# Optimization experiments

Measured on AMD Instinct MI355X. Metric: run time of the kernel, lower is better.

## Reference

```python
import jax, jax.numpy as jnp
import numpy as np

B, S, D, H = 2, 2048, 1024, 16
DK = D // H


def setup_inputs() -> dict:
    key = jax.random.key(0)
    ks = jax.random.split(key, 12)
    sc = 0.02
    inp = {
        "q": jax.random.normal(ks[0], (B, S, D), jnp.float32),
        "k": jax.random.normal(ks[1], (B, S, D), jnp.float32),
        "v": jax.random.normal(ks[2], (B, S, D), jnp.float32),
        "mask": jnp.ones((B, S, S), jnp.int32),
        "Wq": jax.random.normal(ks[3], (D, D), jnp.float32) * sc,
        "bq": jnp.zeros((D,), jnp.float32),
        "Wk": jax.random.normal(ks[4], (D, D), jnp.float32) * sc,
        "bk": jnp.zeros((D,), jnp.float32),
        "Wv": jax.random.normal(ks[5], (D, D), jnp.float32) * sc,
        "bv": jnp.zeros((D,), jnp.float32),
        "Wo": jax.random.normal(ks[6], (D, D), jnp.float32) * sc,
        "bo": jnp.zeros((D,), jnp.float32),
    }
    return inp


def _split_heads(x):
    # [B,S,D] -> [B,H,S,DK]
    b, s, _ = x.shape
    return x.reshape(b, s, H, DK).transpose(0, 2, 1, 3)


def reference(q, k, v, mask, Wq, bq, Wk, bk, Wv, bv, Wo, bo):
    qh = _split_heads(q @ Wq.T + bq)
    kh = _split_heads(k @ Wk.T + bk)
    vh = _split_heads(v @ Wv.T + bv)
    scale = 1.0 / jnp.sqrt(jnp.float32(DK))
    scores = jnp.einsum("bhqd,bhkd->bhqk", qh, kh) * scale  # [B,H,S,S]
    scores = jnp.where(mask[:, None, :, :] == 0, jnp.float32(-1e9), scores)
    probs = jax.nn.softmax(scores, axis=-1)  # dropout p=0.0 -> identity
    out = jnp.einsum("bhqk,bhkd->bhqd", probs, vh)  # [B,H,S,DK]
    concat = out.transpose(0, 2, 1, 3).reshape(q.shape[0], -1, D)
    return concat @ Wo.T + bo
```

## Files before the change

### kernel.cpp

```cpp
#include <hip/hip_runtime.h>
#include <stdint.h>

#define Bsz 2
#define Ssz 2048
#define Dsz 1024
#define Hsz 16
#define DKsz 64

typedef __attribute__((ext_vector_type(8))) short sh8;
typedef __attribute__((ext_vector_type(4))) float fx4;
typedef __attribute__((ext_vector_type(16))) float fx16;
typedef __attribute__((ext_vector_type(4))) unsigned ux4;

__device__ __forceinline__ unsigned short f2bf(float x) {
  uint32_t u = __builtin_bit_cast(uint32_t, x);
  uint32_t r = (u + 0x7fffu + ((u >> 16) & 1u)) >> 16;
  return (unsigned short)r;
}

__device__ __forceinline__ fx4 mfma16(sh8 a, sh8 b, fx4 c) {
  return __builtin_amdgcn_mfma_f32_16x16x32_bf16(a, b, c, 0, 0, 0);
}

__device__ __forceinline__ fx16 mfma32(sh8 a, sh8 b, fx16 c) {
  return __builtin_amdgcn_mfma_f32_32x32x16_bf16(a, b, c, 0, 0, 0);
}

__device__ __forceinline__ void g2l16(const void* g, void* l) {
  __builtin_amdgcn_global_load_lds((const __attribute__((address_space(1))) void*)g,
                                   (__attribute__((address_space(3))) void*)l, 16, 0, 0);
}

__device__ __forceinline__ float fexp2(float x) {
#if __has_builtin(__builtin_amdgcn_exp2f)
  return __builtin_amdgcn_exp2f(x);
#else
  return exp2f(x);
#endif
}

__device__ __forceinline__ unsigned cvtpk(float lo, float hi) {
  unsigned r;
  asm("v_cvt_pk_bf16_f32 %0, %1, %2" : "=v"(r) : "v"(lo), "v"(hi));
  return r;
}

__device__ __forceinline__ void plswap(unsigned& a, unsigned& b) {
  asm("v_permlane32_swap_b32 %0, %1" : "+v"(a), "+v"(b));
}

__device__ __forceinline__ void build_pa(const fx16& p, sh8& pa0, sh8& pa1) {
  unsigned w0 = cvtpk(p[0], p[1]), w1 = cvtpk(p[2], p[3]);
  unsigned w2 = cvtpk(p[4], p[5]), w3 = cvtpk(p[6], p[7]);
  unsigned w4 = cvtpk(p[8], p[9]), w5 = cvtpk(p[10], p[11]);
  unsigned w6 = cvtpk(p[12], p[13]), w7 = cvtpk(p[14], p[15]);
  plswap(w0, w2);
  plswap(w1, w3);
  ux4 u0 = {w0, w1, w2, w3};
  pa0 = __builtin_bit_cast(sh8, u0);
  plswap(w4, w6);
  plswap(w5, w7);
  ux4 u1 = {w4, w5, w6, w7};
  pa1 = __builtin_bit_cast(sh8, u1);
}

__global__ __launch_bounds__(256) void convert_kernel(
    const float* __restrict__ wq, const float* __restrict__ wk, const float* __restrict__ wv,
    const float* __restrict__ wo, const int* __restrict__ mask,
    unsigned short* __restrict__ wqb, unsigned short* __restrict__ wkb,
    unsigned short* __restrict__ wvb, unsigned short* __restrict__ wob,
    int* __restrict__ flag) {
  const int NW = Dsz * Dsz / 4;
  const int NC = 4 * NW;
  const int NM = Bsz * Ssz * Ssz / 4;
  const int total = NC + NM;
  int bad = 0;
  for (int i = blockIdx.x * blockDim.x + threadIdx.x; i < total; i += gridDim.x * blockDim.x) {
    if (i >= NC) {
      int4 m = ((const int4*)mask)[i - NC];
      if (m.x == 0 || m.y == 0 || m.z == 0 || m.w == 0) bad = 1;
      continue;
    }
    int t = i / NW, off = i - t * NW;
    const float* src = (t == 0) ? wq : ((t == 1) ? wk : ((t == 2) ? wv : wo));
    unsigned short* dst = (t == 0) ? wqb : ((t == 1) ? wkb : ((t == 2) ? wvb : wob));
    float4 x = ((const float4*)src)[off];
    ushort4 o;
    o.x = f2bf(x.x); o.y = f2bf(x.y); o.z = f2bf(x.z); o.w = f2bf(x.w);
    ((ushort4*)dst)[off] = o;
  }
  if (bad) atomicAnd(flag, 0);
}

__global__ __launch_bounds__(256) void proj_qkv_kernel(
    const float* __restrict__ qf, const float* __restrict__ kf, const float* __restrict__ vf,
    const unsigned short* __restrict__ wqb, const unsigned short* __restrict__ wkb,
    const unsigned short* __restrict__ wvb,
    const float* __restrict__ bq, const float* __restrict__ bk, const float* __restrict__ bv,
    unsigned short* __restrict__ qh, unsigned short* __restrict__ kh,
    unsigned short* __restrict__ vt) {
  __shared__ __align__(16) unsigned short SMEM[17408];
  unsigned short* Ts = SMEM;
  const int z = blockIdx.z;
  const float* X = (z == 0) ? qf : ((z == 1) ? kf : vf);
  const unsigned short* W = (z == 0) ? wqb : ((z == 1) ? wkb : wvb);
  const float* bias = (z == 0) ? bq : ((z == 1) ? bk : bv);
  const int m0 = blockIdx.x * 128, n0 = blockIdx.y * 128;
  const int tid = threadIdx.x, lane = tid & 63, wid = tid >> 6;
  const int wm = wid >> 1, wn = wid & 1;
  const int c = lane & 15, g = lane >> 4;
  fx4 acc[4][4] = {};

  auto LOADA = [&](int k0, float4* a) {
#pragma unroll
    for (int i = 0; i < 4; i++) {
      int c4 = i * 256 + tid;
      a[i] = *(const float4*)(X + (size_t)(m0 + (c4 >> 3)) * Dsz + k0 + (c4 & 7) * 4);
    }
  };
  auto WRITEA = [&](const float4* a, unsigned short* As) {
#pragma unroll
    for (int i = 0; i < 4; i++) {
      int c4 = i * 256 + tid;
      uint2 w;
      w.x = cvtpk(a[i].x, a[i].y);
      w.y = cvtpk(a[i].z, a[i].w);
      *(uint2*)&As[(c4 >> 3) * 32 + (c4 & 7) * 4] = w;
    }
  };
  auto G2LB = [&](int k0, unsigned short* Bs) {
#pragma unroll
    for (int i = 0; i < 2; i++) {
      int e = i * 256 + tid;
      g2l16(W + (size_t)(n0 + (e >> 2)) * Dsz + k0 + (e & 3) * 8,
            (char*)Bs + (size_t)(i * 256 + wid * 64) * 16);
    }
  };
  auto COMPUTE = [&](const unsigned short* As, const unsigned short* Bs) {
    sh8 af[4], bfr[4];
#pragma unroll
    for (int m = 0; m < 4; m++)
      af[m] = *(const sh8*)&As[(wm * 64 + m * 16 + c) * 32 + g * 8];
#pragma unroll
    for (int n = 0; n < 4; n++)
      bfr[n] = *(const sh8*)&Bs[(wn * 64 + n * 16 + c) * 32 + g * 8];
#pragma unroll
    for (int m = 0; m < 4; m++)
#pragma unroll
      for (int n = 0; n < 4; n++)
        acc[m][n] = mfma16(af[m], bfr[n], acc[m][n]);
  };

  float4 aA[4], aB[4];
  LOADA(0, aA);
  G2LB(0, SMEM + 8192);
  WRITEA(aA, SMEM);
  __syncthreads();
#pragma unroll 1
  for (int j = 0; j < 16; j++) {
    const int k0 = j * 64;
    if (k0 + 32 < Dsz) { LOADA(k0 + 32, aB); G2LB(k0 + 32, SMEM + 12288); }
    COMPUTE(SMEM, SMEM + 8192);
    if (k0 + 32 < Dsz) WRITEA(aB, SMEM + 4096);
    __syncthreads();
    if (k0 + 64 < Dsz) { LOADA(k0 + 64, aA); G2LB(k0 + 64, SMEM + 8192); }
    if (k0 + 32 < Dsz) COMPUTE(SMEM + 4096, SMEM + 12288);
    if (k0 + 64 < Dsz) WRITEA(aA, SMEM);
    __syncthreads();
  }

  const float CE = 0.18033688011112042f;
  if (z < 2) {
    unsigned short* O = (z == 0) ? qh : kh;
    const float sc = (z == 0) ? CE : 1.0f;
#pragma unroll
    for (int n = 0; n < 4; n++) {
      int j = n0 + wn * 64 + n * 16 + c;
      float bj = bias[j];
      int h = j >> 6, dk = j & 63;
#pragma unroll
      for (int m = 0; m < 4; m++)
#pragma unroll
        for (int r = 0; r < 4; r++) {
          int i = m0 + wm * 64 + m * 16 + g * 4 + r;
          int b = i >> 11, s = i & 2047;
          O[(((size_t)(b * Hsz + h) * Ssz + s) << 6) + dk] = f2bf((acc[m][n][r] + bj) * sc);
        }
    }
  } else {
#pragma unroll
    for (int n = 0; n < 4; n++) {
      int nl = wn * 64 + n * 16 + c;
      float bj = bias[n0 + nl];
#pragma unroll
      for (int m = 0; m < 4; m++)
#pragma unroll
        for (int r = 0; r < 4; r++) {
          int ml = wm * 64 + m * 16 + g * 4 + r;
          Ts[nl * 136 + ml] = f2bf(acc[m][n][r] + bj);
        }
    }
    __syncthreads();
    int b = m0 >> 11, sbase = m0 & 2047;
#pragma unroll
    for (int it = 0; it < 8; it++) {
      int ch = it * 256 + tid;
      int row = ch >> 4, off = ch & 15;
      sh8 dv = *(const sh8*)&Ts[row * 136 + off * 8];
      int j = n0 + row;
      int h = j >> 6, dk = j & 63;
      *(sh8*)&vt[(size_t)((b * Hsz + h) * DKsz + dk) * Ssz + sbase + off * 8] = dv;
    }
  }
}

__global__ __launch_bounds__(512, 4) void attn_kernel(
    const unsigned short* __restrict__ qh, const unsigned short* __restrict__ kh,
    const unsigned short* __restrict__ vt, const int* __restrict__ mask,
    const int* __restrict__ flag, unsigned short* __restrict__ concat) {
  __shared__ __align__(16) unsigned short SM[2][2][2][4096];
  const int tid = threadIdx.x, lane = tid & 63, wid = tid >> 6;
  const int grp = wid >> 2, w4 = wid & 3;
  const int fid = blockIdx.y * gridDim.x + blockIdx.x;
  const int logical = (fid & 7) * 64 + (fid >> 3);
  const int bh = logical >> 4, qblk = logical & 15;
  const int b = bh >> 4, h = bh & 15;
  const int q0 = qblk * 128 + w4 * 32;
  const int c = lane & 31, hi = lane >> 5;
  const int cs = c & 7;
  const int kvbase = grp * (Ssz / 2);
  const unsigned short* Qb = qh + ((size_t)bh * Ssz + q0) * DKsz;
  const unsigned short* Kb = kh + (size_t)bh * Ssz * DKsz;
  const unsigned short* Vb = vt + (size_t)bh * DKsz * Ssz;
  const int ch0 = w4 * 128 + lane;
  const int ch1 = ch0 + 64;
  const int r0 = ch0 >> 3, sl0 = (ch0 & 7) ^ (r0 & 7);
  const int r1 = ch1 >> 3, sl1 = (ch1 & 7) ^ (r1 & 7);
  const int koff0 = r0 * DKsz + sl0 * 8, koff1 = r1 * DKsz + sl1 * 8;
  const size_t voff0 = (size_t)r0 * Ssz + sl0 * 8, voff1 = (size_t)r1 * Ssz + sl1 * 8;

  sh8 qf[4];
#pragma unroll
  for (int ks = 0; ks < 4; ks++)
    qf[ks] = *(const sh8*)&Qb[(size_t)c * DKsz + ks * 16 + hi * 8];
  const bool allones = (flag[0] != 0);
  float lsum = 0.f;
  fx16 o0 = {}, o1 = {};

  auto STAGE = [&](int bufi, int kv0) {
    const unsigned short* ksrc = Kb + (size_t)kv0 * DKsz;
    char* kdst = (char*)&SM[0][grp][bufi][0] + w4 * 2048;
    g2l16(ksrc + koff0, kdst);
    g2l16(ksrc + koff1, kdst + 1024);
    const unsigned short* vsrc = Vb + kv0;
    char* vdst = (char*)&SM[1][grp][bufi][0] + w4 * 2048;
    g2l16(vsrc + voff0, vdst);
    g2l16(vsrc + voff1, vdst + 1024);
  };

  const int NT = (Ssz / 2) / 64;
  STAGE(0, kvbase);
  asm volatile("s_waitcnt vmcnt(0)" ::: "memory");
  __builtin_amdgcn_s_barrier();
  asm volatile("" ::: "memory");

  for (int t = 0; t < NT; ++t) {
    const int cur = t & 1;
    const int kv0 = kvbase + t * 64;
    if (t + 1 < NT) STAGE(cur ^ 1, kv0 + 64);
    const unsigned short* Kt = &SM[0][grp][cur][0];
    const unsigned short* Vt = &SM[1][grp][cur][0];
    fx16 s0 = {}, s1 = {};
    __builtin_amdgcn_s_setprio(1);
#pragma unroll
    for (int ks = 0; ks < 4; ks++) {
      int sl = (2 * ks + hi) ^ cs;
      sh8 ka = *(const sh8*)&Kt[(c * 8 + sl) * 8];
      sh8 kb2 = *(const sh8*)&Kt[((32 + c) * 8 + sl) * 8];
      s0 = mfma32(ka, qf[ks], s0);
      s1 = mfma32(kb2, qf[ks], s1);
    }
    __builtin_amdgcn_s_setprio(0);
    if (!allones) {
      const int* mrow = mask + ((size_t)b * Ssz + (q0 + c)) * Ssz + kv0;
#pragma unroll
      for (int r = 0; r < 16; r++) {
        int kv = (r & 3) + 8 * (r >> 2) + 4 * hi;
        if (mrow[kv] == 0) s0[r] = -1e9f;
        if (mrow[32 + kv] == 0) s1[r] = -1e9f;
      }
    }
    fx16 p0v, p1v;
#pragma unroll
    for (int r = 0; r < 16; r++) {
      p0v[r] = fexp2(s0[r]);
      p1v[r] = fexp2(s1[r]);
    }
    sh8 pa[4];
    build_pa(p0v, pa[0], pa[1]);
    build_pa(p1v, pa[2], pa[3]);
    __builtin_amdgcn_s_setprio(1);
#pragma unroll
    for (int ks = 0; ks < 4; ks++) {
      int sl = (2 * ks + hi) ^ cs;
      sh8 v0f = *(const sh8*)&Vt[(c * 8 + sl) * 8];
      sh8 v1f = *(const sh8*)&Vt[((32 + c) * 8 + sl) * 8];
      o0 = mfma32(v0f, pa[ks], o0);
      o1 = mfma32(v1f, pa[ks], o1);
    }
    __builtin_amdgcn_s_setprio(0);
    float sm[16];
#pragma unroll
    for (int r = 0; r < 16; r++) sm[r] = p0v[r] + p1v[r];
#pragma unroll
    for (int w = 8; w >= 1; w >>= 1)
#pragma unroll
      for (int r = 0; r < w; r++) sm[r] += sm[r + w];
    lsum += sm[0];
    asm volatile("s_waitcnt vmcnt(0)" ::: "memory");
    __builtin_amdgcn_s_barrier();
    asm volatile("" ::: "memory");
  }

  float* CB = (float*)&SM[0][0][0][0];
  float* CBl = CB + 4 * 32 * 68;
  if (grp == 1) {
#pragma unroll
    for (int k4 = 0; k4 < 4; k4++) {
      fx4 a = {o0[4 * k4], o0[4 * k4 + 1], o0[4 * k4 + 2], o0[4 * k4 + 3]};
      *(fx4*)&CB[(w4 * 32 + c) * 68 + 8 * k4 + 4 * hi] = a;
      fx4 bvv = {o1[4 * k4], o1[4 * k4 + 1], o1[4 * k4 + 2], o1[4 * k4 + 3]};
      *(fx4*)&CB[(w4 * 32 + c) * 68 + 32 + 8 * k4 + 4 * hi] = bvv;
    }
    CBl[w4 * 64 + hi * 32 + c] = lsum;
  }
  __syncthreads();
  if (grp == 0) {
#pragma unroll
    for (int k4 = 0; k4 < 4; k4++) {
      fx4 a = *(const fx4*)&CB[(w4 * 32 + c) * 68 + 8 * k4 + 4 * hi];
      o0[4 * k4] += a[0]; o0[4 * k4 + 1] += a[1]; o0[4 * k4 + 2] += a[2]; o0[4 * k4 + 3] += a[3];
      fx4 bvv = *(const fx4*)&CB[(w4 * 32 + c) * 68 + 32 + 8 * k4 + 4 * hi];
      o1[4 * k4] += bvv[0]; o1[4 * k4 + 1] += bvv[1]; o1[4 * k4 + 2] += bvv[2]; o1[4 * k4 + 3] += bvv[3];
    }
    lsum += CBl[w4 * 64 + hi * 32 + c];
    lsum += __shfl_xor(lsum, 32);
    float linv = 1.0f / lsum;
    unsigned short* Ob = concat + ((size_t)b * Ssz + q0 + c) * Dsz + h * DKsz;
#pragma unroll
    for (int rg = 0; rg < 4; rg++) {
      ushort4 w;
      w.x = f2bf(o0[rg * 4 + 0] * linv);
      w.y = f2bf(o0[rg * 4 + 1] * linv);
      w.z = f2bf(o0[rg * 4 + 2] * linv);
      w.w = f2bf(o0[rg * 4 + 3] * linv);
      *(ushort4*)&Ob[8 * rg + 4 * hi] = w;
      ushort4 w2;
      w2.x = f2bf(o1[rg * 4 + 0] * linv);
      w2.y = f2bf(o1[rg * 4 + 1] * linv);
      w2.z = f2bf(o1[rg * 4 + 2] * linv);
      w2.w = f2bf(o1[rg * 4 + 3] * linv);
      *(ushort4*)&Ob[32 + 8 * rg + 4 * hi] = w2;
    }
  }
}

__global__ __launch_bounds__(256) void outproj_kernel(
    const unsigned short* __restrict__ Xc, const unsigned short* __restrict__ wob,
    const float* __restrict__ bo, float* __restrict__ out) {
  __shared__ __align__(16) unsigned short As[128 * 32];
  __shared__ __align__(16) unsigned short Bs[128 * 32];
  const int m0 = blockIdx.x * 128, n0 = blockIdx.y * 128;
  const int tid = threadIdx.x, lane = tid & 63, wid = tid >> 6;
  const int wm = wid >> 1, wn = wid & 1;
  const int c = lane & 15, g = lane >> 4;
  fx4 acc[4][4] = {};
  for (int k0 = 0; k0 < Dsz; k0 += 32) {
#pragma unroll
    for (int i = 0; i < 2; i++) {
      int e = i * 256 + tid;
      g2l16(Xc + (size_t)(m0 + (e >> 2)) * Dsz + k0 + (e & 3) * 8,
            (char*)As + (size_t)(i * 256 + wid * 64) * 16);
      g2l16(wob + (size_t)(n0 + (e >> 2)) * Dsz + k0 + (e & 3) * 8,
            (char*)Bs + (size_t)(i * 256 + wid * 64) * 16);
    }
    __syncthreads();
    sh8 af[4], bfr[4];
#pragma unroll
    for (int m = 0; m < 4; m++)
      af[m] = *(const sh8*)&As[(wm * 64 + m * 16 + c) * 32 + g * 8];
#pragma unroll
    for (int n = 0; n < 4; n++)
      bfr[n] = *(const sh8*)&Bs[(wn * 64 + n * 16 + c) * 32 + g * 8];
#pragma unroll
    for (int m = 0; m < 4; m++)
#pragma unroll
      for (int n = 0; n < 4; n++)
        acc[m][n] = mfma16(af[m], bfr[n], acc[m][n]);
    __syncthreads();
  }
#pragma unroll
  for (int n = 0; n < 4; n++) {
    int j = n0 + wn * 64 + n * 16 + c;
    float bj = bo[j];
#pragma unroll
    for (int m = 0; m < 4; m++)
#pragma unroll
      for (int r = 0; r < 4; r++) {
        int i = m0 + wm * 64 + m * 16 + g * 4 + r;
        out[(size_t)i * Dsz + j] = acc[m][n][r] + bj;
      }
  }
}

extern "C" void kernel_launch(void* const* d_in, const int* in_sizes, int n_in,
                              void* d_out, int out_size, void* d_ws, size_t ws_size,
                              hipStream_t stream) {
  const float* q = (const float*)d_in[0];
  const float* k = (const float*)d_in[1];
  const float* v = (const float*)d_in[2];
  const int* mask = (const int*)d_in[3];
  const float* Wq = (const float*)d_in[4];
  const float* bq = (const float*)d_in[5];
  const float* Wk = (const float*)d_in[6];
  const float* bk = (const float*)d_in[7];
  const float* Wv = (const float*)d_in[8];
  const float* bv = (const float*)d_in[9];
  const float* Wo = (const float*)d_in[10];
  const float* bo = (const float*)d_in[11];
  float* out = (float*)d_out;
  char* ws = (char*)d_ws;
  const size_t MB = 1 << 20;
  unsigned short* wqb = (unsigned short*)(ws + 0 * MB);
  unsigned short* wkb = (unsigned short*)(ws + 2 * MB);
  unsigned short* wvb = (unsigned short*)(ws + 4 * MB);
  unsigned short* wob = (unsigned short*)(ws + 6 * MB);
  unsigned short* qhp = (unsigned short*)(ws + 8 * MB);
  unsigned short* khp = (unsigned short*)(ws + 16 * MB);
  unsigned short* vtp = (unsigned short*)(ws + 24 * MB);
  unsigned short* cc  = (unsigned short*)(ws + 32 * MB);
  int* flag = (int*)(ws + 40 * MB);

  hipMemsetAsync(flag, 0xFF, 4, stream);
  hipLaunchKernelGGL(convert_kernel, dim3(1024), dim3(256), 0, stream,
                     Wq, Wk, Wv, Wo, mask, wqb, wkb, wvb, wob, flag);
  hipLaunchKernelGGL(proj_qkv_kernel, dim3(32, 8, 3), dim3(256), 0, stream,
                     q, k, v, wqb, wkb, wvb, bq, bk, bv, qhp, khp, vtp);
  hipLaunchKernelGGL(attn_kernel, dim3(16, 32), dim3(512), 0, stream,
                     qhp, khp, vtp, mask, flag, cc);
  hipLaunchKernelGGL(outproj_kernel, dim3(32, 8), dim3(256), 0, stream,
                     cc, wob, bo, out);
}
```

Baseline: 139.0 us.

## Halve attention KV tile to 32 and raise occupancy to 8 blocks per CU

Shrinks the per-iteration KV tile from 64 to 32 keys, which halves the score and P fragments and the LDS staging per buffer, re-swizzles the V tile for a 32-wide row, and raises launch bounds to 8 blocks per SM. The aim is lower register and LDS pressure so more waves can hide latency. The cost is twice as many loop iterations, each with its own barrier and wait, and less MFMA work between synchronisations. The unified LDS array is sized so the epilogue reduction buffer still fits.

```diff
diff --git a/kernel.cpp b/kernel.cpp
--- a/kernel.cpp
+++ b/kernel.cpp
@@ -214,11 +214,11 @@
   }
 }
 
-__global__ __launch_bounds__(512, 4) void attn_kernel(
+__global__ __launch_bounds__(512, 8) void attn_kernel(
     const unsigned short* __restrict__ qh, const unsigned short* __restrict__ kh,
     const unsigned short* __restrict__ vt, const int* __restrict__ mask,
     const int* __restrict__ flag, unsigned short* __restrict__ concat) {
-  __shared__ __align__(16) unsigned short SM[2][2][2][4096];
+  __shared__ __align__(16) unsigned short SMEM[17920];
   const int tid = threadIdx.x, lane = tid & 63, wid = tid >> 6;
   const int grp = wid >> 2, w4 = wid & 3;
   const int fid = blockIdx.y * gridDim.x + blockIdx.x;
@@ -227,17 +227,15 @@
   const int b = bh >> 4, h = bh & 15;
   const int q0 = qblk * 128 + w4 * 32;
   const int c = lane & 31, hi = lane >> 5;
-  const int cs = c & 7;
   const int kvbase = grp * (Ssz / 2);
   const unsigned short* Qb = qh + ((size_t)bh * Ssz + q0) * DKsz;
   const unsigned short* Kb = kh + (size_t)bh * Ssz * DKsz;
   const unsigned short* Vb = vt + (size_t)bh * DKsz * Ssz;
-  const int ch0 = w4 * 128 + lane;
-  const int ch1 = ch0 + 64;
-  const int r0 = ch0 >> 3, sl0 = (ch0 & 7) ^ (r0 & 7);
-  const int r1 = ch1 >> 3, sl1 = (ch1 & 7) ^ (r1 & 7);
-  const int koff0 = r0 * DKsz + sl0 * 8, koff1 = r1 * DKsz + sl1 * 8;
-  const size_t voff0 = (size_t)r0 * Ssz + sl0 * 8, voff1 = (size_t)r1 * Ssz + sl1 * 8;
+  const int chk = w4 * 64 + lane;
+  const int krow = chk >> 3, ksl = (chk & 7) ^ (krow & 7);
+  const int koff = krow * DKsz + ksl * 8;
+  const int vrow = chk >> 2, vsl = (chk & 3) ^ (vrow & 3);
+  const size_t voff = (size_t)vrow * Ssz + vsl * 8;
 
   sh8 qf[4];
 #pragma unroll
@@ -248,17 +246,12 @@
   fx16 o0 = {}, o1 = {};
 
   auto STAGE = [&](int bufi, int kv0) {
-    const unsigned short* ksrc = Kb + (size_t)kv0 * DKsz;
-    char* kdst = (char*)&SM[0][grp][bufi][0] + w4 * 2048;
-    g2l16(ksrc + koff0, kdst);
-    g2l16(ksrc + koff1, kdst + 1024);
-    const unsigned short* vsrc = Vb + kv0;
-    char* vdst = (char*)&SM[1][grp][bufi][0] + w4 * 2048;
-    g2l16(vsrc + voff0, vdst);
-    g2l16(vsrc + voff1, vdst + 1024);
+    unsigned short* base = SMEM + grp * 8192 + bufi * 4096;
+    g2l16(Kb + (size_t)kv0 * DKsz + koff, (char*)base + w4 * 1024);
+    g2l16(Vb + kv0 + voff, (char*)(base + 2048) + w4 * 1024);
   };
 
-  const int NT = (Ssz / 2) / 64;
+  const int NT = (Ssz / 2) / 32;
   STAGE(0, kvbase);
   asm volatile("s_waitcnt vmcnt(0)" ::: "memory");
   __builtin_amdgcn_s_barrier();
@@ -266,19 +259,17 @@
 
   for (int t = 0; t < NT; ++t) {
     const int cur = t & 1;
-    const int kv0 = kvbase + t * 64;
-    if (t + 1 < NT) STAGE(cur ^ 1, kv0 + 64);
-    const unsigned short* Kt = &SM[0][grp][cur][0];
-    const unsigned short* Vt = &SM[1][grp][cur][0];
-    fx16 s0 = {}, s1 = {};
+    const int kv0 = kvbase + t * 32;
+    if (t + 1 < NT) STAGE(cur ^ 1, kv0 + 32);
+    const unsigned short* Kt = SMEM + grp * 8192 + cur * 4096;
+    const unsigned short* Vt = Kt + 2048;
+    fx16 s0 = {};
     __builtin_amdgcn_s_setprio(1);
 #pragma unroll
     for (int ks = 0; ks < 4; ks++) {
-      int sl = (2 * ks + hi) ^ cs;
-      sh8 ka = *(const sh8*)&Kt[(c * 8 + sl) * 8];
-      sh8 kb2 = *(const sh8*)&Kt[((32 + c) * 8 + sl) * 8];
+      int sl = (2 * ks + hi) ^ (c & 7);
+      sh8 ka = *(const sh8*)&Kt[c * 64 + sl * 8];
       s0 = mfma32(ka, qf[ks], s0);
-      s1 = mfma32(kb2, qf[ks], s1);
     }
     __builtin_amdgcn_s_setprio(0);
     if (!allones) {
@@ -287,33 +278,32 @@
       for (int r = 0; r < 16; r++) {
         int kv = (r & 3) + 8 * (r >> 2) + 4 * hi;
         if (mrow[kv] == 0) s0[r] = -1e9f;
-        if (mrow[32 + kv] == 0) s1[r] = -1e9f;
       }
     }
-    fx16 p0v, p1v;
-#pragma unroll
-    for (int r = 0; r < 16; r++) {
-      p0v[r] = fexp2(s0[r]);
-      p1v[r] = fexp2(s1[r]);
-    }
-    sh8 pa[4];
-    build_pa(p0v, pa[0], pa[1]);
-    build_pa(p1v, pa[2], pa[3]);
+    fx16 p0v;
+#pragma unroll
+    for (int r = 0; r < 16; r++) p0v[r] = fexp2(s0[r]);
+    sh8 pa0, pa1;
+    build_pa(p0v, pa0, pa1);
     __builtin_amdgcn_s_setprio(1);
-#pragma unroll
-    for (int ks = 0; ks < 4; ks++) {
-      int sl = (2 * ks + hi) ^ cs;
-      sh8 v0f = *(const sh8*)&Vt[(c * 8 + sl) * 8];
-      sh8 v1f = *(const sh8*)&Vt[((32 + c) * 8 + sl) * 8];
-      o0 = mfma32(v0f, pa[ks], o0);
-      o1 = mfma32(v1f, pa[ks], o1);
+    {
+      int sl0 = (0 * 2 + hi), sl1 = (1 * 2 + hi);
+      int rd0 = c, rd1 = 32 + c;
+      sh8 va = *(const sh8*)&Vt[rd0 * 32 + (sl0 ^ (rd0 & 3)) * 8];
+      sh8 vb2 = *(const sh8*)&Vt[rd1 * 32 + (sl0 ^ (rd1 & 3)) * 8];
+      o0 = mfma32(va, pa0, o0);
+      o1 = mfma32(vb2, pa0, o1);
+      va = *(const sh8*)&Vt[rd0 * 32 + (sl1 ^ (rd0 & 3)) * 8];
+      vb2 = *(const sh8*)&Vt[rd1 * 32 + (sl1 ^ (rd1 & 3)) * 8];
+      o0 = mfma32(va, pa1, o0);
+      o1 = mfma32(vb2, pa1, o1);
     }
     __builtin_amdgcn_s_setprio(0);
-    float sm[16];
-#pragma unroll
-    for (int r = 0; r < 16; r++) sm[r] = p0v[r] + p1v[r];
-#pragma unroll
-    for (int w = 8; w >= 1; w >>= 1)
+    float sm[8];
+#pragma unroll
+    for (int r = 0; r < 8; r++) sm[r] = p0v[r] + p0v[r + 8];
+#pragma unroll
+    for (int w = 4; w >= 1; w >>= 1)
 #pragma unroll
       for (int r = 0; r < w; r++) sm[r] += sm[r + w];
     lsum += sm[0];
@@ -322,7 +312,7 @@
     asm volatile("" ::: "memory");
   }
 
-  float* CB = (float*)&SM[0][0][0][0];
+  float* CB = (float*)&SMEM[0];
   float* CBl = CB + 4 * 32 * 68;
   if (grp == 1) {
 #pragma unroll
```

After: 524.0 us. 277% more time.
